# Performance work log

Measured on AMD Instinct MI355X. Metric: run time of the kernel, lower is better.

The kernel has to match this reference:

```python
import jax, jax.numpy as jnp
import numpy as np

GAMMA = 1.0        # soft-min temperature for differentiable DTW
BIG = 1e9          # value for cells outside the Sakoe-Chiba band
DTW_BW = 0.2       # band width as fraction of normalized path deviation
AVG_T_LEN = True   # divide discrepancy by input sequence length


def _softmin3(a, b, c):
    # differentiable min over the three DP predecessors
    z = jnp.stack([a, b, c], axis=0)
    return -GAMMA * jax.nn.logsumexp(-z / GAMMA, axis=0)


def _dtw(C, mask):
    """Band-limited soft-DTW DP. C: [T,K] pairwise costs, mask: [T,K] bool band.
    Returns scalar D[T-1,K-1]. Row scan over T; inner scan over K carries the
    left neighbor (recurrence D[i,j] = C[i,j] + softmin(D[i-1,j], D[i,j-1], D[i-1,j-1]))."""
    T, K = C.shape

    def row_step(carry, inp):
        prev_row, diag0 = carry            # prev_row: D[i-1,:]; diag0: virtual D[i-1,-1]
        c_row, m_row = inp
        diag = jnp.concatenate([diag0[None], prev_row[:-1]])  # D[i-1,j-1]

        def col_step(left, xs):
            c, up, dg, m = xs
            d = c + _softmin3(up, left, dg)
            d = jnp.where(m, d, BIG)       # kill cells outside the band
            return d, d

        _, row = jax.lax.scan(col_step, jnp.float32(BIG), (c_row, prev_row, diag, m_row))
        return (row, jnp.float32(BIG)), None

    # virtual border: D[-1,-1] = 0, all other border cells = BIG
    init = (jnp.full((K,), BIG, dtype=jnp.float32), jnp.float32(0.0))
    (last_row, _), _ = jax.lax.scan(row_step, init, (C, mask))
    return last_row[-1]


def setup_inputs() -> dict:
    key = jax.random.key(0)
    kx, kp = jax.random.split(key)
    B, T = 64, 512
    F, K = 32, 64
    x = jax.random.normal(kx, (B, T), dtype=jnp.float32)
    protos = jax.random.normal(kp, (F, K), dtype=jnp.float32)  # learnable DTW kernels
    return {"x": x, "protos": protos}


def reference(x, protos):
    B, T = x.shape
    F, K = protos.shape
    # pairwise squared costs: [B, F, T, K]
    C = (x[:, None, :, None] - protos[None, :, None, :]) ** 2
    # Sakoe-Chiba band on normalized coordinates
    ii = jnp.arange(T, dtype=jnp.float32) / (T - 1)
    jj = jnp.arange(K, dtype=jnp.float32) / (K - 1)
    mask = jnp.abs(ii[:, None] - jj[None, :]) <= DTW_BW  # [T, K]
    d = jax.vmap(jax.vmap(lambda c: _dtw(c, mask)))(C)    # [B, F]
    if AVG_T_LEN:
        d = d / jnp.float32(T)
    return d[:, :, None]  # [B, num_filter, out_len=1]
```

## Files before the change

kernel.cpp:

```cpp
#include <hip/hip_runtime.h>

#define T_LEN  512
#define K_LEN  64
#define NFILT  32
#define NBATCH 64
#define XOFS   64
#define XS_SZ  656
#define CHUNK  32
#define SQRT_LOG2E 1.2011224087864498f
#define LN2        0.6931471805599453f

typedef __attribute__((ext_vector_type(2))) float f32x2;

static __device__ __forceinline__ float wave_shr1(float x) {
    int r = __builtin_amdgcn_update_dpp(0, __builtin_bit_cast(int, x),
                                        0x138, 0xF, 0xF, true);
    return __builtin_bit_cast(float, r);
}

static __device__ __forceinline__ f32x2 wave_shr1_x2(f32x2 v) {
    f32x2 r;
    r.x = wave_shr1(v.x);
    r.y = wave_shr1(v.y);
    return r;
}

template <int N>
static __device__ __forceinline__ float row_ror(float x) {
    int r = __builtin_amdgcn_update_dpp(0, __builtin_bit_cast(int, x),
                                        0x120 + N, 0xF, 0xF, true);
    return __builtin_bit_cast(float, r);
}

static __device__ __forceinline__ float exp2_fast(float x) {
#if __has_builtin(__builtin_amdgcn_exp2f)
    return __builtin_amdgcn_exp2f(x);
#else
    return exp2f(x);
#endif
}

__global__ __launch_bounds__(256) void dtw_kernel(const float* __restrict__ x,
                                                  const float* __restrict__ protos,
                                                  float* __restrict__ out) {
    __shared__ float xs[XS_SZ];
    const int tid  = threadIdx.x;
    const int lane = tid & 63;
    const int wid  = tid >> 6;
    const int b    = blockIdx.x >> 2;
    const int fA   = ((blockIdx.x & 3) << 2) | wid;
    const int fB   = fA + 16;

    for (int t0 = tid; t0 < XS_SZ; t0 += 256) {
        int i = t0 - XOFS;
        xs[t0] = (i >= 0 && i < T_LEN) ? x[b * T_LEN + i] * SQRT_LOG2E : 0.0f;
    }
    __syncthreads();

    const float pAn = -protos[fA * K_LEN + lane] * SQRT_LOG2E;
    const float pBn = -protos[fB * K_LEN + lane] * SQRT_LOG2E;
    const float jj  = (float)lane / 63.0f;

    int a0 = 0, b0 = T_LEN - 1;
    while (a0 < b0) { int m = (a0 + b0) >> 1;
        if ((float)m / 511.0f - jj >= -0.2f) b0 = m; else a0 = m + 1; }
    const int ilo = a0;
    a0 = 0; b0 = T_LEN - 1;
    while (a0 < b0) { int m = (a0 + b0 + 1) >> 1;
        if ((float)m / 511.0f - jj <= 0.2f) a0 = m; else b0 = m - 1; }
    const int ihi = a0;

    const unsigned range = (unsigned)(ihi - ilo);
    unsigned t = (unsigned)(-(lane + ilo));
    f32x2 prev2 = {0.0f, 0.0f};
    const float d0 = (lane == 0) ? 1.0f : 0.0f;
    f32x2 dgp2 = {d0, d0};
    int   S2A = 0, S2B = 0;

    const float* __restrict__ xp = &xs[XOFS - lane];

    float xr[8];
#pragma unroll
    for (int i = 0; i < 8; ++i) xr[i] = xp[i];

#define STEP(CB, S) do {                                      \
        float xv_  = xr[(S) & 7];                             \
        xr[(S) & 7] = xp[(CB) + (S) + 8];                     \
        float sel_ = (t <= range) ? 0.0f : -3.0e38f;          \
        ++t;                                                  \
        float dA_ = xv_ + pAn;                                \
        float dB_ = xv_ + pBn;                                \
        f32x2 w2_;                                            \
        w2_.x = exp2_fast(__builtin_fmaf(dA_, -dA_, sel_));   \
        w2_.y = exp2_fast(__builtin_fmaf(dB_, -dB_, sel_));   \
        f32x2 l2_ = wave_shr1_x2(prev2);                      \
        f32x2 a2_ = prev2 + dgp2;                             \
        f32x2 s2_ = a2_ + l2_;                                \
        dgp2  = l2_;                                          \
        prev2 = s2_ * w2_;                                    \
    } while (0)

#define RENORM_HALF(PVE, DGE, S2) do {                                       \
        float m_ = prev2.PVE;                                                \
        m_ = fmaxf(m_, row_ror<8>(m_));                                      \
        m_ = fmaxf(m_, row_ror<4>(m_));                                      \
        m_ = fmaxf(m_, row_ror<2>(m_));                                      \
        m_ = fmaxf(m_, row_ror<1>(m_));                                      \
        int mi_ = __builtin_bit_cast(int, m_);                               \
        unsigned r0_ = (unsigned)__builtin_amdgcn_readlane(mi_, 0);          \
        unsigned r1_ = (unsigned)__builtin_amdgcn_readlane(mi_, 16);         \
        unsigned r2_ = (unsigned)__builtin_amdgcn_readlane(mi_, 32);         \
        unsigned r3_ = (unsigned)__builtin_amdgcn_readlane(mi_, 48);         \
        unsigned ra_ = r0_ > r1_ ? r0_ : r1_;                                \
        unsigned rb_ = r2_ > r3_ ? r2_ : r3_;                                \
        unsigned mx_ = ra_ > rb_ ? ra_ : rb_;                                \
        int e_  = (int)((mx_ >> 23) & 0xFF);                                 \
        int Me_ = 284 - e_;                                                  \
        Me_ = Me_ < 1 ? 1 : (Me_ > 254 ? 254 : Me_);                         \
        float M_ = __builtin_bit_cast(float, Me_ << 23);                     \
        S2 += Me_ - 127;                                                     \
        prev2.PVE *= M_;                                                     \
        dgp2.DGE  *= M_;                                                     \
    } while (0)

#define RENORM() do { RENORM_HALF(x, x, S2A); RENORM_HALF(y, y, S2B); } while (0)

#pragma unroll 1
    for (int c = 0; c < 17; ++c) {
        const int cb = c * CHUNK;
#pragma unroll
        for (int s = 0; s < CHUNK; ++s) STEP(cb, s);
        RENORM();
    }
#pragma unroll
    for (int s = 0; s < 31; ++s) STEP(544, s);

    if (lane == 63) {
        float DA = ((float)S2A - log2f(prev2.x)) * LN2;
        float DB = ((float)S2B - log2f(prev2.y)) * LN2;
        out[b * NFILT + fA] = DA * (1.0f / (float)T_LEN);
        out[b * NFILT + fB] = DB * (1.0f / (float)T_LEN);
    }
#undef STEP
#undef RENORM_HALF
#undef RENORM
}

extern "C" void kernel_launch(void* const* d_in, const int* in_sizes, int n_in,
                              void* d_out, int out_size, void* d_ws, size_t ws_size,
                              hipStream_t stream) {
    const float* x      = (const float*)d_in[0];
    const float* protos = (const float*)d_in[1];
    float* out          = (float*)d_out;

    dim3 grid(NBATCH * 4);
    dim3 block(256);
    hipLaunchKernelGGL(dtw_kernel, grid, block, 0, stream, x, protos, out);
}
```

Baseline: 28.53 us.

## Split soft-DTW into forward and backward halves meeting at the middle row

Runs the wavefront DP from both ends at once: a forward pass over the first half of the rows and a backward pass over the reversed second half, then joins them by summing forward times backward products across the meeting row. This roughly halves the serial dependency chain (about 287 instead of 575 anti-diagonal steps) while doubling per-step work, which may be cheap because of ILP. It also replaces the per-step LDS reload ring with double-buffered 32-element register chunks. The risks are higher register pressure and numerical scaling mismatches at the join.

Result: slower. 54.27 us (+90.2%).

```diff
diff --git a/kernel.cpp b/kernel.cpp
--- a/kernel.cpp
+++ b/kernel.cpp
@@ -4,9 +4,8 @@
 #define K_LEN  64
 #define NFILT  32
 #define NBATCH 64
-#define XOFS   64
-#define XS_SZ  656
-#define CHUNK  32
+#define XOFS2  64
+#define XS2_SZ 384
 #define SQRT_LOG2E 1.2011224087864498f
 #define LN2        0.6931471805599453f
 
@@ -40,10 +39,21 @@
 #endif
 }
 
+static __device__ __forceinline__ void band_iv(float jj, int& lo, int& hi) {
+    int a0 = 0, b0 = T_LEN - 1;
+    while (a0 < b0) { int m = (a0 + b0) >> 1;
+        if ((float)m / 511.0f - jj >= -0.2f) b0 = m; else a0 = m + 1; }
+    lo = a0;
+    a0 = 0; b0 = T_LEN - 1;
+    while (a0 < b0) { int m = (a0 + b0 + 1) >> 1;
+        if ((float)m / 511.0f - jj <= 0.2f) a0 = m; else b0 = m - 1; }
+    hi = a0;
+}
+
 __global__ __launch_bounds__(256) void dtw_kernel(const float* __restrict__ x,
                                                   const float* __restrict__ protos,
                                                   float* __restrict__ out) {
-    __shared__ float xs[XS_SZ];
+    __shared__ f32x2 xs2[XS2_SZ];
     const int tid  = threadIdx.x;
     const int lane = tid & 63;
     const int wid  = tid >> 6;
@@ -51,57 +61,85 @@
     const int fA   = ((blockIdx.x & 3) << 2) | wid;
     const int fB   = fA + 16;
 
-    for (int t0 = tid; t0 < XS_SZ; t0 += 256) {
-        int i = t0 - XOFS;
-        xs[t0] = (i >= 0 && i < T_LEN) ? x[b * T_LEN + i] * SQRT_LOG2E : 0.0f;
+    for (int t0 = tid; t0 < XS2_SZ; t0 += 256) {
+        int i = t0 - XOFS2;
+        f32x2 v;
+        bool ok = (i >= 0 && i < T_LEN);
+        v.x = ok ? x[b * T_LEN + i] * SQRT_LOG2E : 0.0f;
+        v.y = ok ? x[b * T_LEN + (T_LEN - 1) - i] * SQRT_LOG2E : 0.0f;
+        xs2[t0] = v;
     }
     __syncthreads();
 
-    const float pAn = -protos[fA * K_LEN + lane] * SQRT_LOG2E;
-    const float pBn = -protos[fB * K_LEN + lane] * SQRT_LOG2E;
-    const float jj  = (float)lane / 63.0f;
-
-    int a0 = 0, b0 = T_LEN - 1;
-    while (a0 < b0) { int m = (a0 + b0) >> 1;
-        if ((float)m / 511.0f - jj >= -0.2f) b0 = m; else a0 = m + 1; }
-    const int ilo = a0;
-    a0 = 0; b0 = T_LEN - 1;
-    while (a0 < b0) { int m = (a0 + b0 + 1) >> 1;
-        if ((float)m / 511.0f - jj <= 0.2f) a0 = m; else b0 = m - 1; }
-    const int ihi = a0;
-
-    const unsigned range = (unsigned)(ihi - ilo);
-    unsigned t = (unsigned)(-(lane + ilo));
-    f32x2 prev2 = {0.0f, 0.0f};
+    const int jF = lane, jB = 63 - lane;
+    f32x2 pnF2, pnB2;
+    pnF2.x = -protos[fA * K_LEN + jF] * SQRT_LOG2E;
+    pnF2.y = -protos[fB * K_LEN + jF] * SQRT_LOG2E;
+    pnB2.x = -protos[fA * K_LEN + jB] * SQRT_LOG2E;
+    pnB2.y = -protos[fB * K_LEN + jB] * SQRT_LOG2E;
+
+    int iloF, ihiF, iloB, ihiB;
+    band_iv((float)jF / 63.0f, iloF, ihiF);
+    band_iv((float)jB / 63.0f, iloB, ihiB);
+
+    const int loF = iloF, hiF = (ihiF < 255) ? ihiF : 255;
+    const int loBo = (iloB > 256) ? iloB : 256;
+    const int loB  = (T_LEN - 1) - ihiB;
+    const int hiB  = (T_LEN - 1) - loBo;
+
+    unsigned tF, rangeF, tB, rangeB;
+    if (loF > hiF) { tF = 0x80000000u; rangeF = 0u; }
+    else { tF = (unsigned)(-(lane + loF)); rangeF = (unsigned)(hiF - loF); }
+    if (loB > hiB) { tB = 0x80000000u; rangeB = 0u; }
+    else { tB = (unsigned)(-(lane + loB)); rangeB = (unsigned)(hiB - loB); }
+
+    f32x2 prevF2 = {0.0f, 0.0f}, prevB2 = {0.0f, 0.0f};
+    f32x2 capF2  = {0.0f, 0.0f}, capB2  = {0.0f, 0.0f};
     const float d0 = (lane == 0) ? 1.0f : 0.0f;
-    f32x2 dgp2 = {d0, d0};
-    int   S2A = 0, S2B = 0;
-
-    const float* __restrict__ xp = &xs[XOFS - lane];
-
-    float xr[8];
+    f32x2 dgpF2 = {d0, d0}, dgpB2 = {d0, d0};
+    int S2FA = 0, S2FB = 0, S2BA = 0, S2BB = 0;
+    const int dcap = 255 + lane;
+
+    const f32x2* __restrict__ xp = &xs2[XOFS2 - lane];
+
+    f32x2 A[32], Bv[32];
 #pragma unroll
-    for (int i = 0; i < 8; ++i) xr[i] = xp[i];
-
-#define STEP(CB, S) do {                                      \
-        float xv_  = xr[(S) & 7];                             \
-        xr[(S) & 7] = xp[(CB) + (S) + 8];                     \
-        float sel_ = (t <= range) ? 0.0f : -3.0e38f;          \
-        ++t;                                                  \
-        float dA_ = xv_ + pAn;                                \
-        float dB_ = xv_ + pBn;                                \
-        f32x2 w2_;                                            \
-        w2_.x = exp2_fast(__builtin_fmaf(dA_, -dA_, sel_));   \
-        w2_.y = exp2_fast(__builtin_fmaf(dB_, -dB_, sel_));   \
-        f32x2 l2_ = wave_shr1_x2(prev2);                      \
-        f32x2 a2_ = prev2 + dgp2;                             \
-        f32x2 s2_ = a2_ + l2_;                                \
-        dgp2  = l2_;                                          \
-        prev2 = s2_ * w2_;                                    \
-    } while (0)
-
-#define RENORM_HALF(PVE, DGE, S2) do {                                       \
-        float m_ = prev2.PVE;                                                \
+    for (int k = 0; k < 32; ++k) A[k] = xp[k];
+    __builtin_amdgcn_sched_barrier(0);
+
+#define STEP(XV, DCONST, CAPF) do {                           \
+        f32x2 xv2_ = (XV);                                    \
+        float selF_ = (tF <= rangeF) ? 0.0f : -3.0e38f; ++tF; \
+        float selB_ = (tB <= rangeB) ? 0.0f : -3.0e38f; ++tB; \
+        float dFA_ = xv2_.x + pnF2.x;                         \
+        float dFB_ = xv2_.x + pnF2.y;                         \
+        float dBA_ = xv2_.y + pnB2.x;                         \
+        float dBB_ = xv2_.y + pnB2.y;                         \
+        f32x2 wF_, wB_;                                       \
+        wF_.x = exp2_fast(__builtin_fmaf(dFA_, -dFA_, selF_));\
+        wF_.y = exp2_fast(__builtin_fmaf(dFB_, -dFB_, selF_));\
+        wB_.x = exp2_fast(__builtin_fmaf(dBA_, -dBA_, selB_));\
+        wB_.y = exp2_fast(__builtin_fmaf(dBB_, -dBB_, selB_));\
+        f32x2 lF_ = wave_shr1_x2(prevF2);                     \
+        f32x2 lB_ = wave_shr1_x2(prevB2);                     \
+        f32x2 aF_ = prevF2 + dgpF2;                           \
+        f32x2 aB_ = prevB2 + dgpB2;                           \
+        f32x2 sF_ = aF_ + lF_;                                \
+        f32x2 sB_ = aB_ + lB_;                                \
+        dgpF2 = lF_; dgpB2 = lB_;                             \
+        prevF2 = sF_ * wF_;                                   \
+        prevB2 = sB_ * wB_;                                   \
+        if (CAPF) {                                           \
+            bool c_ = (dcap == (DCONST));                     \
+            capF2.x = c_ ? prevF2.x : capF2.x;                \
+            capF2.y = c_ ? prevF2.y : capF2.y;                \
+            capB2.x = c_ ? prevB2.x : capB2.x;                \
+            capB2.y = c_ ? prevB2.y : capB2.y;                \
+        }                                                     \
+    } while (0)
+
+#define RENORM_CH(PV, DG, CP, S2, TGT) do {                                  \
+        float m_ = PV;                                                       \
         m_ = fmaxf(m_, row_ror<8>(m_));                                      \
         m_ = fmaxf(m_, row_ror<4>(m_));                                      \
         m_ = fmaxf(m_, row_ror<2>(m_));                                      \
@@ -115,35 +153,84 @@
         unsigned rb_ = r2_ > r3_ ? r2_ : r3_;                                \
         unsigned mx_ = ra_ > rb_ ? ra_ : rb_;                                \
         int e_  = (int)((mx_ >> 23) & 0xFF);                                 \
-        int Me_ = 284 - e_;                                                  \
+        int Me_ = (TGT) - e_;                                                \
         Me_ = Me_ < 1 ? 1 : (Me_ > 254 ? 254 : Me_);                         \
         float M_ = __builtin_bit_cast(float, Me_ << 23);                     \
         S2 += Me_ - 127;                                                     \
-        prev2.PVE *= M_;                                                     \
-        dgp2.DGE  *= M_;                                                     \
-    } while (0)
-
-#define RENORM() do { RENORM_HALF(x, x, S2A); RENORM_HALF(y, y, S2B); } while (0)
-
-#pragma unroll 1
-    for (int c = 0; c < 17; ++c) {
-        const int cb = c * CHUNK;
+        PV *= M_;                                                            \
+        DG *= M_;                                                            \
+        CP *= M_;                                                            \
+    } while (0)
+
+#define RENORM() do {                                                        \
+        RENORM_CH(prevF2.x, dgpF2.x, capF2.x, S2FA, 284);                    \
+        RENORM_CH(prevF2.y, dgpF2.y, capF2.y, S2FB, 284);                    \
+        RENORM_CH(prevB2.x, dgpB2.x, capB2.x, S2BA, 284);                    \
+        RENORM_CH(prevB2.y, dgpB2.y, capB2.y, S2BB, 284);                    \
+    } while (0)
+
+#define CHUNKRUN(CBASE, CUR, NXT, CAPF) do {                                 \
+        _Pragma("unroll")                                                    \
+        for (int k = 0; k < 32; ++k) NXT[k] = xp[(CBASE) + 32 + k];          \
+        __builtin_amdgcn_sched_barrier(0);                                   \
+        _Pragma("unroll")                                                    \
+        for (int k = 0; k < 32; ++k) STEP(CUR[k], (CBASE) + k, CAPF);        \
+        RENORM();                                                            \
+        __builtin_amdgcn_sched_barrier(0);                                   \
+    } while (0)
+
+    CHUNKRUN(  0, A,  Bv, 0);
+    CHUNKRUN( 32, Bv, A,  0);
+    CHUNKRUN( 64, A,  Bv, 0);
+    CHUNKRUN( 96, Bv, A,  0);
+    CHUNKRUN(128, A,  Bv, 0);
+    CHUNKRUN(160, Bv, A,  0);
+    CHUNKRUN(192, A,  Bv, 0);
+    CHUNKRUN(224, Bv, A,  1);
+    CHUNKRUN(256, A,  Bv, 1);
 #pragma unroll
-        for (int s = 0; s < CHUNK; ++s) STEP(cb, s);
-        RENORM();
-    }
-#pragma unroll
-    for (int s = 0; s < 31; ++s) STEP(544, s);
+    for (int k = 0; k < 31; ++k) STEP(Bv[k], 288 + k, 1);
+
+    RENORM_CH(capF2.x, dgpF2.x, prevF2.x, S2FA, 254);
+    RENORM_CH(capF2.y, dgpF2.y, prevF2.y, S2FB, 254);
+    RENORM_CH(capB2.x, dgpB2.x, prevB2.x, S2BA, 254);
+    RENORM_CH(capB2.y, dgpB2.y, prevB2.y, S2BB, 254);
+
+    float cbjA  = __shfl(capB2.x, 63 - lane);
+    float cbj1A = __shfl(capB2.x, 62 - lane);
+    float cbjB  = __shfl(capB2.y, 63 - lane);
+    float cbj1B = __shfl(capB2.y, 62 - lane);
+    float sA = capF2.x * (cbjA + cbj1A);
+    float sB = capF2.y * (cbjB + cbj1B);
+
+    float mA = sA;
+    mA += row_ror<8>(mA); mA += row_ror<4>(mA);
+    mA += row_ror<2>(mA); mA += row_ror<1>(mA);
+    int miA = __builtin_bit_cast(int, mA);
+    float totA = mA;
+    totA += __builtin_bit_cast(float, __builtin_amdgcn_readlane(miA, 0));
+    totA += __builtin_bit_cast(float, __builtin_amdgcn_readlane(miA, 16));
+    totA += __builtin_bit_cast(float, __builtin_amdgcn_readlane(miA, 32));
+
+    float mB = sB;
+    mB += row_ror<8>(mB); mB += row_ror<4>(mB);
+    mB += row_ror<2>(mB); mB += row_ror<1>(mB);
+    int miB = __builtin_bit_cast(int, mB);
+    float totB = mB;
+    totB += __builtin_bit_cast(float, __builtin_amdgcn_readlane(miB, 0));
+    totB += __builtin_bit_cast(float, __builtin_amdgcn_readlane(miB, 16));
+    totB += __builtin_bit_cast(float, __builtin_amdgcn_readlane(miB, 32));
 
     if (lane == 63) {
-        float DA = ((float)S2A - log2f(prev2.x)) * LN2;
-        float DB = ((float)S2B - log2f(prev2.y)) * LN2;
+        float DA = ((float)(S2FA + S2BA) - log2f(totA)) * LN2;
+        float DB = ((float)(S2FB + S2BB) - log2f(totB)) * LN2;
         out[b * NFILT + fA] = DA * (1.0f / (float)T_LEN);
         out[b * NFILT + fB] = DB * (1.0f / (float)T_LEN);
     }
 #undef STEP
-#undef RENORM_HALF
+#undef RENORM_CH
 #undef RENORM
+#undef CHUNKRUN
 }
 
 extern "C" void kernel_launch(void* const* d_in, const int* in_sizes, int n_in,
```
